# Kernel tuning notes

Measured on AMD Instinct MI355X. Metric: run time of the kernel, lower is better.

## Reference

```python
import jax, jax.numpy as jnp
import numpy as np

S, N, DIN, DH, C, K, E = 12, 50000, 64, 128, 2, 3, 600000
HID = (DH + C) // 2  # 65
LN_EPS = 1e-5


def setup_inputs() -> dict:
    key = jax.random.key(0)
    ks = jax.random.split(key, 16)
    sc = 0.05
    inp = {
        'H': jax.random.normal(ks[0], (S, N, DIN), dtype=jnp.float32),
        'edge_index': jax.random.randint(ks[1], (2, E), 0, N, dtype=jnp.int64),
        # stacked gate params, gate order: 0=i, 1=f, 2=c(cell), 3=o
        'Wx': jax.random.normal(ks[2], (4, K, DIN, DH), dtype=jnp.float32) * sc,
        'bx': jnp.zeros((4, DH), dtype=jnp.float32),
        'Wh': jax.random.normal(ks[3], (4, K, DH, DH), dtype=jnp.float32) * sc,
        'bh': jnp.zeros((4, DH), dtype=jnp.float32),
        'b_gate': jnp.zeros((4, DH), dtype=jnp.float32),
        'wc': jax.random.normal(ks[4], (3, DH), dtype=jnp.float32) * sc,  # peephole: i, f, o
        'ln_gamma': jnp.ones((DH,), dtype=jnp.float32),
        'ln_beta': jnp.zeros((DH,), dtype=jnp.float32),
        'W1': jax.random.normal(ks[5], (DH, HID), dtype=jnp.float32) * sc,
        'b1': jnp.zeros((HID,), dtype=jnp.float32),
        'W2': jax.random.normal(ks[6], (HID, C), dtype=jnp.float32) * sc,
        'b2': jnp.zeros((C,), dtype=jnp.float32),
    }
    return inp


def _cheb_norm(edge_index):
    # sym-normalized, lambda_max=2 => scaled Laplacian Lhat = -D^-1/2 A D^-1/2 (zero diagonal)
    src, dst = edge_index[0], edge_index[1]
    ones = jnp.ones((src.shape[0],), dtype=jnp.float32)
    deg = jax.ops.segment_sum(ones, src, num_segments=N)
    dinv = jnp.where(deg > 0, jax.lax.rsqrt(jnp.maximum(deg, 1.0)), 0.0)
    norm = -dinv[src] * dinv[dst]
    return src, dst, norm


def _cheb_conv(x, W, b, src, dst, norm):
    # x: [N, Din]; W: [K, Din, Dout]. T0=x, T1=Lhat x, Tk=2 Lhat T_{k-1} - T_{k-2}
    Tx0 = x
    out = Tx0 @ W[0]
    if K > 1:
        Tx1 = jax.ops.segment_sum(norm[:, None] * Tx0[src], dst, num_segments=N)
        out = out + Tx1 @ W[1]
        for k in range(2, K):
            Tx2 = 2.0 * jax.ops.segment_sum(norm[:, None] * Tx1[src], dst, num_segments=N) - Tx0
            out = out + Tx2 @ W[k]
            Tx0, Tx1 = Tx1, Tx2
    return out + b


def _decoder(H, edge_index, Wx, bx, Wh, bh, b_gate, wc, ln_gamma, ln_beta, W1, b1, W2, b2):
    src, dst, norm = _cheb_norm(edge_index)

    def step(carry, x_t):
        h, c = carry
        gx = lambda g: _cheb_conv(x_t, Wx[g], bx[g], src, dst, norm)
        gh = lambda g: _cheb_conv(h, Wh[g], bh[g], src, dst, norm)
        i = jax.nn.sigmoid(gx(0) + gh(0) + wc[0] * c + b_gate[0])
        f = jax.nn.sigmoid(gx(1) + gh(1) + wc[1] * c + b_gate[1])
        t = jnp.tanh(gx(2) + gh(2) + b_gate[2])
        c = f * c + i * t
        o = jax.nn.sigmoid(gx(3) + gh(3) + wc[2] * c + b_gate[3])
        h = o * jnp.tanh(c)
        return (h, c), h

    h0 = jnp.zeros((N, DH), dtype=H.dtype)
    (_, _), X = jax.lax.scan(step, (h0, h0), H)  # X: [S, N, DH]

    X = jnp.tanh(X)
    # LayerNorm over conv_dim (last axis here)
    mu = jnp.mean(X, axis=-1, keepdims=True)
    var = jnp.mean(jnp.square(X - mu), axis=-1, keepdims=True)
    X = (X - mu) * jax.lax.rsqrt(var + LN_EPS) * ln_gamma + ln_beta
    # dropout in eval mode: identity
    X = jax.nn.relu(X @ W1 + b1) @ W2 + b2  # [S, N, C]
    X = jax.nn.sigmoid(X)
    return jnp.transpose(X, (1, 2, 0))  # [N, C, S]


def reference(H, edge_index, Wx, bx, Wh, bh, b_gate, wc, ln_gamma, ln_beta, W1, b1, W2, b2):
    return _decoder(H, edge_index, Wx, bx, Wh, bh, b_gate, wc, ln_gamma, ln_beta, W1, b1, W2, b2)
```

## Files before the change

kernel.cpp:

```cpp
#include <hip/hip_runtime.h>
#include <cstdint>
#include <cstddef>

#define S_DIM 12
#define N_NODE 50000
#define N_PAD 50048
#define N_P2 50176
#define D_IN 64
#define D_H 128
#define N_E 600000
#define K_TOT 576
#define N_COL 512
#define HID_P 80
#define N_HID 65
#define AXC 192

#define NB_PREP 1152
#define NB_DEG 2344
#define NB_SPMM 12500
#define NB_LN 782

typedef short bf16x8 __attribute__((ext_vector_type(8)));
typedef float f32x4 __attribute__((ext_vector_type(4)));

__device__ __forceinline__ float bf2f(unsigned short u){
  union { unsigned int i; float f; } v; v.i = ((unsigned int)u) << 16; return v.f;
}
__device__ __forceinline__ unsigned short f2bf(float f){
  union { float f; unsigned int i; } v; v.f = f;
  unsigned int x = v.i;
  return (unsigned short)((x + 0x7fffu + ((x >> 16) & 1u)) >> 16);
}
__device__ __forceinline__ float sigf(float x){ return 1.f/(1.f + __expf(-x)); }
__device__ __forceinline__ float ftanh(float x){
  x = fminf(fmaxf(x, -12.f), 12.f);
  float e = __expf(2.f*x);
  return (e - 1.f)/(e + 1.f);
}
__device__ __forceinline__ void gload16(const void* g, void* lds){
  __builtin_amdgcn_global_load_lds((const __attribute__((address_space(1))) unsigned int*)g,
                                   (__attribute__((address_space(3))) unsigned int*)lds, 16, 0, 0);
}
__device__ __forceinline__ void acc6(float* a, unsigned int p0, unsigned int p1, unsigned int p2, float w){
  unsigned int u[3] = {p0, p1, p2};
#pragma unroll
  for (int i=0;i<3;++i){
    a[2*i]   += w * bf2f((unsigned short)(u[i] & 0xffffu));
    a[2*i+1] += w * bf2f((unsigned short)(u[i] >> 16));
  }
}
__device__ __forceinline__ void acc8(float* a, uint4 h, float w){
  unsigned int u[4] = {h.x, h.y, h.z, h.w};
#pragma unroll
  for (int i=0;i<4;++i){
    a[2*i]   += w * bf2f((unsigned short)(u[i] & 0xffffu));
    a[2*i+1] += w * bf2f((unsigned short)(u[i] >> 16));
  }
}

__global__ void k_setup(const int* __restrict__ ei,
                        const float* __restrict__ Wx, const float* __restrict__ Wh,
                        const float* __restrict__ bx, const float* __restrict__ bh,
                        const float* __restrict__ bg, const float* __restrict__ W1,
                        const float* __restrict__ b1, const float* __restrict__ W2,
                        unsigned short* __restrict__ Bct, float* __restrict__ btot,
                        unsigned short* __restrict__ W1t, float* __restrict__ b1p,
                        float* __restrict__ W2p,
                        int* __restrict__ dsrc, int* __restrict__ ddst)
{
  int bb = blockIdx.x, tid = threadIdx.x;
  if (bb < NB_PREP){
    int idx = bb*256 + tid;
    if (idx < N_COL*K_TOT){
      int cc = idx / K_TOT, k = idx - cc*K_TOT;
      int g = (cc>>4)&3, d = (cc&15) + ((cc>>6)<<4);
      float v;
      if (k < 384){
        int kt = k >> 7, j = k & 127;
        const float* Wg = Wh + (size_t)g*3*128*128;
        if (kt == 0)      v = Wg[(size_t)j*128 + d] - Wg[(size_t)(256+j)*128 + d];
        else if (kt == 1) v = Wg[(size_t)(128+j)*128 + d];
        else              v = 2.f*Wg[(size_t)(256+j)*128 + d];
      } else {
        int kk = k - 384; int kt = kk >> 6, j = kk & 63;
        const float* Wg = Wx + (size_t)g*3*64*128;
        if (kt == 0)      v = Wg[(size_t)j*128 + d] - Wg[(size_t)(128+j)*128 + d];
        else if (kt == 1) v = Wg[(size_t)(64+j)*128 + d];
        else              v = 2.f*Wg[(size_t)(128+j)*128 + d];
      }
      Bct[(size_t)cc*K_TOT + k] = f2bf(v);
    }
    if (idx < N_COL) btot[idx] = bx[idx] + bh[idx] + bg[idx];
    if (idx < HID_P*D_H){ int c = idx >> 7, k = idx & 127;
      W1t[idx] = (c < N_HID) ? f2bf(W1[k*N_HID + c]) : (unsigned short)0; }
    if (idx < HID_P) b1p[idx] = (idx < N_HID) ? b1[idx] : 0.f;
    if (idx < HID_P*2){ int c = idx >> 1, j = idx & 1; W2p[idx] = (c < N_HID) ? W2[c*2 + j] : 0.f; }
  } else {
    int e = (bb - NB_PREP)*256 + tid;
    if (e < N_E){
      atomicAdd(&dsrc[ei[e]], 1);
      atomicAdd(&ddst[ei[N_E + e]], 1);
    }
  }
}

__global__ void k_xprep(const float* __restrict__ H, unsigned short* __restrict__ Xtr,
                        unsigned short* __restrict__ Axt)
{
  int idx = blockIdx.x*256 + threadIdx.x;
  if (idx >= N_PAD*32) return;
  int n = idx >> 5, d0 = (idx & 31)*2;
  unsigned int pk[12];
  if (n < N_NODE){
    const float* hp = H + (size_t)n*64 + d0;
#pragma unroll
    for (int t=0;t<12;++t){
      float2 v = *(const float2*)(hp + (size_t)t*N_NODE*64);
      pk[t] = (unsigned int)f2bf(v.x) | ((unsigned int)f2bf(v.y) << 16);
    }
  } else {
#pragma unroll
    for (int t=0;t<12;++t) pk[t] = 0;
  }
#pragma unroll
  for (int t=0;t<12;++t)
    *(unsigned int*)(Axt + ((size_t)t*N_PAD + n)*AXC + d0) = pk[t];
  if (n >= N_NODE){
#pragma unroll
    for (int t=0;t<12;++t){
      *(unsigned int*)(Axt + ((size_t)t*N_PAD + n)*AXC + 64  + d0) = 0;
      *(unsigned int*)(Axt + ((size_t)t*N_PAD + n)*AXC + 128 + d0) = 0;
    }
  }
  unsigned int* c0  = (unsigned int*)(Xtr + ((size_t)n*64 + d0)*6);
  unsigned int* c1  = (unsigned int*)(Xtr + ((size_t)n*64 + d0 + 1)*6);
  unsigned int* c0b = (unsigned int*)(Xtr + (size_t)N_PAD*384 + ((size_t)n*64 + d0)*6);
  unsigned int* c1b = (unsigned int*)(Xtr + (size_t)N_PAD*384 + ((size_t)n*64 + d0 + 1)*6);
#pragma unroll
  for (int i=0;i<3;++i){
    c0[i]  = (pk[2*i]   & 0xffffu) | (pk[2*i+1]   << 16);
    c1[i]  = (pk[2*i]   >> 16)     | (pk[2*i+1]   & 0xffff0000u);
    c0b[i] = (pk[6+2*i] & 0xffffu) | (pk[6+2*i+1] << 16);
    c1b[i] = (pk[6+2*i] >> 16)     | (pk[6+2*i+1] & 0xffff0000u);
  }
}

__global__ void k_scan1d(const int* __restrict__ in, int* __restrict__ outp, int* __restrict__ part,
                         const int* __restrict__ dsrc, float* __restrict__ dinv){
  __shared__ int sm[256];
  int tid = threadIdx.x;
  int i = blockIdx.x*256 + tid;
  dinv[i] = (dsrc[i] > 0) ? rsqrtf((float)dsrc[i]) : 0.f;
  int v = in[i];
  int x = v;
  sm[tid] = x; __syncthreads();
  for (int off=1; off<256; off<<=1){
    int y = (tid >= off) ? sm[tid-off] : 0;
    __syncthreads();
    x += y; sm[tid] = x; __syncthreads();
  }
  outp[i] = x - v;
  if (tid == 255) part[blockIdx.x] = x;
}
__global__ void k_scan2(int* __restrict__ part, int nblk){
  __shared__ int sm[256];
  int tid = threadIdx.x;
  int v = (tid < nblk) ? part[tid] : 0;
  int x = v; sm[tid] = x; __syncthreads();
  for (int off=1; off<256; off<<=1){
    int y = (tid >= off) ? sm[tid-off] : 0;
    __syncthreads();
    x += y; sm[tid] = x; __syncthreads();
  }
  if (tid < nblk) part[tid] = x - v;
}
__global__ void k_scan3(const int* __restrict__ outp, const int* __restrict__ part, int* __restrict__ offs){
  int i = blockIdx.x*256 + threadIdx.x;
  offs[i] = outp[i] + part[blockIdx.x];
}
__global__ void k_csr(const int* __restrict__ ei, const float* __restrict__ dinv,
                      const int* __restrict__ offs, int* __restrict__ cursor,
                      int2* __restrict__ cedge){
  int e = blockIdx.x*256 + threadIdx.x;
  if (e < N_E){
    int s = ei[e], d = ei[N_E + e];
    int pos = atomicAdd(&cursor[d], 1);
    float w = -dinv[s]*dinv[d];
    cedge[offs[d] + pos] = make_int2(s, __float_as_int(w));
  }
}

__global__ void k_xspmm1(const unsigned short* __restrict__ Xh, unsigned short* __restrict__ AxtH,
                         unsigned short* __restrict__ Uh,
                         const int* __restrict__ offs, const int2* __restrict__ cedge){
  int n = blockIdx.x*4 + (threadIdx.x >> 6);
  int l = threadIdx.x & 63;
  if (n >= N_NODE) return;
  int beg = offs[n], end = offs[n+1];
  int ce = end - 1;
  float a[6];
#pragma unroll
  for (int t=0;t<6;++t) a[t] = 0.f;
  for (int q = beg; q < end; q += 6){
    int2 e0 = cedge[min(q,   ce)];
    int2 e1 = cedge[min(q+1, ce)];
    int2 e2 = cedge[min(q+2, ce)];
    int2 e3 = cedge[min(q+3, ce)];
    int2 e4 = cedge[min(q+4, ce)];
    int2 e5 = cedge[min(q+5, ce)];
    float w0 = __int_as_float(e0.y);
    float w1 = (q+1 < end) ? __int_as_float(e1.y) : 0.f;
    float w2 = (q+2 < end) ? __int_as_float(e2.y) : 0.f;
    float w3 = (q+3 < end) ? __int_as_float(e3.y) : 0.f;
    float w4 = (q+4 < end) ? __int_as_float(e4.y) : 0.f;
    float w5 = (q+5 < end) ? __int_as_float(e5.y) : 0.f;
    const unsigned int* r0 = (const unsigned int*)(Xh + ((size_t)e0.x*64 + l)*6);
    const unsigned int* r1 = (const unsigned int*)(Xh + ((size_t)e1.x*64 + l)*6);
    const unsigned int* r2 = (const unsigned int*)(Xh + ((size_t)e2.x*64 + l)*6);
    const unsigned int* r3 = (const unsigned int*)(Xh + ((size_t)e3.x*64 + l)*6);
    const unsigned int* r4 = (const unsigned int*)(Xh + ((size_t)e4.x*64 + l)*6);
    const unsigned int* r5 = (const unsigned int*)(Xh + ((size_t)e5.x*64 + l)*6);
    unsigned int p00=r0[0], p01=r0[1], p02=r0[2];
    unsigned int p10=r1[0], p11=r1[1], p12=r1[2];
    unsigned int p20=r2[0], p21=r2[1], p22=r2[2];
    unsigned int p30=r3[0], p31=r3[1], p32=r3[2];
    unsigned int p40=r4[0], p41=r4[1], p42=r4[2];
    unsigned int p50=r5[0], p51=r5[1], p52=r5[2];
    acc6(a, p00, p01, p02, w0);
    acc6(a, p10, p11, p12, w1);
    acc6(a, p20, p21, p22, w2);
    acc6(a, p30, p31, p32, w3);
    acc6(a, p40, p41, p42, w4);
    acc6(a, p50, p51, p52, w5);
  }
  unsigned short u[6];
#pragma unroll
  for (int t=0;t<6;++t){
    u[t] = f2bf(a[t]);
    AxtH[((size_t)t*N_PAD + n)*AXC + 64 + l] = u[t];
  }
  unsigned int* op = (unsigned int*)(Uh + ((size_t)n*64 + l)*6);
#pragma unroll
  for (int i=0;i<3;++i) op[i] = (unsigned int)u[2*i] | ((unsigned int)u[2*i+1] << 16);
}
__global__ void k_xspmm2(const unsigned short* __restrict__ Uh, unsigned short* __restrict__ AxtH,
                         const int* __restrict__ offs, const int2* __restrict__ cedge){
  int n = blockIdx.x*4 + (threadIdx.x >> 6);
  int l = threadIdx.x & 63;
  if (n >= N_NODE) return;
  int beg = offs[n], end = offs[n+1];
  int ce = end - 1;
  float a[6];
#pragma unroll
  for (int t=0;t<6;++t) a[t] = 0.f;
  for (int q = beg; q < end; q += 6){
    int2 e0 = cedge[min(q,   ce)];
    int2 e1 = cedge[min(q+1, ce)];
    int2 e2 = cedge[min(q+2, ce)];
    int2 e3 = cedge[min(q+3, ce)];
    int2 e4 = cedge[min(q+4, ce)];
    int2 e5 = cedge[min(q+5, ce)];
    float w0 = __int_as_float(e0.y);
    float w1 = (q+1 < end) ? __int_as_float(e1.y) : 0.f;
    float w2 = (q+2 < end) ? __int_as_float(e2.y) : 0.f;
    float w3 = (q+3 < end) ? __int_as_float(e3.y) : 0.f;
    float w4 = (q+4 < end) ? __int_as_float(e4.y) : 0.f;
    float w5 = (q+5 < end) ? __int_as_float(e5.y) : 0.f;
    const unsigned int* r0 = (const unsigned int*)(Uh + ((size_t)e0.x*64 + l)*6);
    const unsigned int* r1 = (const unsigned int*)(Uh + ((size_t)e1.x*64 + l)*6);
    const unsigned int* r2 = (const unsigned int*)(Uh + ((size_t)e2.x*64 + l)*6);
    const unsigned int* r3 = (const unsigned int*)(Uh + ((size_t)e3.x*64 + l)*6);
    const unsigned int* r4 = (const unsigned int*)(Uh + ((size_t)e4.x*64 + l)*6);
    const unsigned int* r5 = (const unsigned int*)(Uh + ((size_t)e5.x*64 + l)*6);
    unsigned int p00=r0[0], p01=r0[1], p02=r0[2];
    unsigned int p10=r1[0], p11=r1[1], p12=r1[2];
    unsigned int p20=r2[0], p21=r2[1], p22=r2[2];
    unsigned int p30=r3[0], p31=r3[1], p32=r3[2];
    unsigned int p40=r4[0], p41=r4[1], p42=r4[2];
    unsigned int p50=r5[0], p51=r5[1], p52=r5[2];
    acc6(a, p00, p01, p02, w0);
    acc6(a, p10, p11, p12, w1);
    acc6(a, p20, p21, p22, w2);
    acc6(a, p30, p31, p32, w3);
    acc6(a, p40, p41, p42, w4);
    acc6(a, p50, p51, p52, w5);
  }
#pragma unroll
  for (int t=0;t<6;++t)
    AxtH[((size_t)t*N_PAD + n)*AXC + 128 + l] = f2bf(a[t]);
}

__device__ __forceinline__ void spmm1_body(int n, int l,
    const unsigned short* __restrict__ Hc, unsigned short* __restrict__ U,
    const int* __restrict__ offs, const int2* __restrict__ cedge)
{
  if (n >= N_NODE) return;
  int sub = l >> 4, fl = l & 15;
  int beg = offs[n], end = offs[n+1];
  int ce = end - 1;
  float a[8];
#pragma unroll
  for (int j=0;j<8;++j) a[j] = 0.f;
  for (int q = beg; q < end; q += 16){
    int i0 = q + sub, i1 = q + 4 + sub, i2 = q + 8 + sub, i3 = q + 12 + sub;
    int2 e0 = cedge[min(i0, ce)];
    int2 e1 = cedge[min(i1, ce)];
    int2 e2 = cedge[min(i2, ce)];
    int2 e3 = cedge[min(i3, ce)];
    float w0 = (i0 < end) ? __int_as_float(e0.y) : 0.f;
    float w1 = (i1 < end) ? __int_as_float(e1.y) : 0.f;
    float w2 = (i2 < end) ? __int_as_float(e2.y) : 0.f;
    float w3 = (i3 < end) ? __int_as_float(e3.y) : 0.f;
    uint4 h0 = *(const uint4*)(Hc + (size_t)e0.x*128 + fl*8);
    uint4 h1 = *(const uint4*)(Hc + (size_t)e1.x*128 + fl*8);
    uint4 h2 = *(const uint4*)(Hc + (size_t)e2.x*128 + fl*8);
    uint4 h3 = *(const uint4*)(Hc + (size_t)e3.x*128 + fl*8);
    acc8(a, h0, w0);
    acc8(a, h1, w1);
    acc8(a, h2, w2);
    acc8(a, h3, w3);
  }
#pragma unroll
  for (int j=0;j<8;++j){
    a[j] += __shfl_xor(a[j], 16);
    a[j] += __shfl_xor(a[j], 32);
  }
  if (sub == 0){
    unsigned short o[8];
#pragma unroll
    for (int j=0;j<8;++j) o[j] = f2bf(a[j]);
    *(uint4*)(U + (size_t)n*256 + fl*8) = *(const uint4*)o;
  }
}

__global__ void k_spmm2(unsigned short* __restrict__ U,
                        const int* __restrict__ offs, const int2* __restrict__ cedge){
  int n = blockIdx.x*4 + (threadIdx.x >> 6);
  int l = threadIdx.x & 63;
  if (n >= N_NODE) return;
  int sub = l >> 4, fl = l & 15;
  int beg = offs[n], end = offs[n+1];
  int ce = end - 1;
  float a[8];
#pragma unroll
  for (int j=0;j<8;++j) a[j] = 0.f;
  for (int q = beg; q < end; q += 16){
    int i0 = q + sub, i1 = q + 4 + sub, i2 = q + 8 + sub, i3 = q + 12 + sub;
    int2 e0 = cedge[min(i0, ce)];
    int2 e1 = cedge[min(i1, ce)];
    int2 e2 = cedge[min(i2, ce)];
    int2 e3 = cedge[min(i3, ce)];
    float w0 = (i0 < end) ? __int_as_float(e0.y) : 0.f;
    float w1 = (i1 < end) ? __int_as_float(e1.y) : 0.f;
    float w2 = (i2 < end) ? __int_as_float(e2.y) : 0.f;
    float w3 = (i3 < end) ? __int_as_float(e3.y) : 0.f;
    uint4 h0 = *(const uint4*)(U + (size_t)e0.x*256 + fl*8);
    uint4 h1 = *(const uint4*)(U + (size_t)e1.x*256 + fl*8);
    uint4 h2 = *(const uint4*)(U + (size_t)e2.x*256 + fl*8);
    uint4 h3 = *(const uint4*)(U + (size_t)e3.x*256 + fl*8);
    acc8(a, h0, w0);
    acc8(a, h1, w1);
    acc8(a, h2, w2);
    acc8(a, h3, w3);
  }
#pragma unroll
  for (int j=0;j<8;++j){
    a[j] += __shfl_xor(a[j], 16);
    a[j] += __shfl_xor(a[j], 32);
  }
  if (sub == 0){
    unsigned short o[8];
#pragma unroll
    for (int j=0;j<8;++j) o[j] = f2bf(a[j]);
    *(uint4*)(U + (size_t)n*256 + 128 + fl*8) = *(const uint4*)o;
  }
}

__device__ __forceinline__ void lnmlp_body(int n0,
    const unsigned short* __restrict__ Hn,
    const unsigned short* __restrict__ W1t, const float* __restrict__ b1p,
    const float* __restrict__ W2p, const float* __restrict__ b2,
    const float* __restrict__ gam, const float* __restrict__ bet,
    float* __restrict__ out, int t)
{
  __shared__ __align__(16) unsigned short xn[64*128];
  __shared__ __align__(16) unsigned short w1s[HID_P*128];
  __shared__ float w2s[HID_P*2];
  __shared__ float b1s[HID_P];
  __shared__ float b2s[2];
  int tid = threadIdx.x;
  for (int i = tid; i < HID_P*128/8; i += 256) ((int4*)w1s)[i] = ((const int4*)W1t)[i];
  if (tid < HID_P*2) w2s[tid] = W2p[tid];
  if (tid < HID_P)   b1s[tid] = b1p[tid];
  if (tid < 2)       b2s[tid] = b2[tid];
  int row = tid >> 2, part = tid & 3;
  int n = n0 + row;
  float vals[32];
  float s = 0.f, ss = 0.f;
  if (n < N_NODE){
    const unsigned short* hp = Hn + (size_t)n*128 + part*32;
#pragma unroll
    for (int k=0;k<32;++k){
      float x = ftanh(bf2f(hp[k]));
      vals[k] = x; s += x; ss += x*x;
    }
  } else {
#pragma unroll
    for (int k=0;k<32;++k) vals[k] = 0.f;
  }
  s  += __shfl_xor(s,1);  s  += __shfl_xor(s,2);
  ss += __shfl_xor(ss,1); ss += __shfl_xor(ss,2);
  float mu = s * (1.f/128.f);
  float var = ss * (1.f/128.f) - mu*mu;
  float inv = rsqrtf(fmaxf(var, 0.f) + 1e-5f);
#pragma unroll
  for (int k=0;k<32;++k){
    int d = part*32 + k;
    xn[row*128 + d] = f2bf((vals[k]-mu)*inv*gam[d] + bet[d]);
  }
  __syncthreads();
  int w = tid >> 6, l = tid & 63;
  const f32x4 vzero = {0.f,0.f,0.f,0.f};
  f32x4 acc[5];
#pragma unroll
  for (int tj=0;tj<5;++tj) acc[tj] = vzero;
#pragma unroll
  for (int kk=0;kk<4;++kk){
    bf16x8 a = *(const bf16x8*)(xn + (w*16 + (l&15))*128 + kk*32 + (l>>4)*8);
#pragma unroll
    for (int tj=0;tj<5;++tj){
      bf16x8 b = *(const bf16x8*)(w1s + (tj*16 + (l&15))*128 + kk*32 + (l>>4)*8);
      acc[tj] = __builtin_amdgcn_mfma_f32_16x16x32_bf16(a, b, acc[tj], 0,0,0);
    }
  }
#pragma unroll
  for (int r=0;r<4;++r){
    int rn = n0 + w*16 + (l>>4)*4 + r;
    float p0 = 0.f, p1 = 0.f;
#pragma unroll
    for (int tj=0;tj<5;++tj){
      int col = tj*16 + (l&15);
      float hv = fmaxf(acc[tj][r] + b1s[col], 0.f);
      p0 += hv * w2s[col*2];
      p1 += hv * w2s[col*2+1];
    }
    p0 += __shfl_xor(p0,1); p0 += __shfl_xor(p0,2); p0 += __shfl_xor(p0,4); p0 += __shfl_xor(p0,8);
    p1 += __shfl_xor(p1,1); p1 += __shfl_xor(p1,2); p1 += __shfl_xor(p1,4); p1 += __shfl_xor(p1,8);
    if ((l & 15) == 0 && rn < N_NODE){
      float* op = out + (size_t)rn*24 + t;
      op[0]  = sigf(p0 + b2s[0]);
      op[12] = sigf(p1 + b2s[1]);
    }
  }
}

__global__ void k_sp1ln(const unsigned short* __restrict__ Hc, unsigned short* __restrict__ U,
                        const int* __restrict__ offs, const int2* __restrict__ cedge,
                        const unsigned short* __restrict__ W1t, const float* __restrict__ b1p,
                        const float* __restrict__ W2p, const float* __restrict__ b2,
                        const float* __restrict__ gam, const float* __restrict__ bet,
                        float* __restrict__ out, int tprev)
{
  int bb = blockIdx.x;
  if (bb < NB_SPMM){
    spmm1_body(bb*4 + (threadIdx.x >> 6), threadIdx.x & 63, Hc, U, offs, cedge);
  } else {
    lnmlp_body((bb - NB_SPMM)*64, Hc, W1t, b1p, W2p, b2, gam, bet, out, tprev);
  }
}

__global__ __launch_bounds__(256,2) void k_lnmlp(const unsigned short* __restrict__ Hn,
                        const unsigned short* __restrict__ W1t, const float* __restrict__ b1p,
                        const float* __restrict__ W2p, const float* __restrict__ b2,
                        const float* __restrict__ gam, const float* __restrict__ bet,
                        float* __restrict__ out, int t)
{
  lnmlp_body(blockIdx.x*64, Hn, W1t, b1p, W2p, b2, gam, bet, out, t);
}

__global__ __launch_bounds__(256,3) void k_gemm(
    const unsigned short* __restrict__ Hc, const unsigned short* __restrict__ U,
    const unsigned short* __restrict__ Axt,
    const unsigned short* __restrict__ Bct, const float* __restrict__ btot,
    const float* __restrict__ wc, float* __restrict__ c, unsigned short* __restrict__ Hn,
    int it0)
{
  int L = blockIdx.y*4 + blockIdx.x;
  int xcd = L & 7, li = L >> 3;
  int by = xcd + ((li >> 2) << 3);
  int bx = li & 3;
  if (by >= N_PAD/128) return;
  __shared__ __align__(16) unsigned short As[128*64];
  __shared__ __align__(16) unsigned short Bs[128*64];
  int tid = threadIdx.x;
  int w = tid >> 6, l = tid & 63;
  int n0 = bx * 128;
  int m0 = by * 128;
  const f32x4 vzero = {0.f,0.f,0.f,0.f};
  f32x4 acc[4][4];
#pragma unroll
  for (int i=0;i<4;++i)
#pragma unroll
    for (int j=0;j<4;++j) acc[i][j] = vzero;
  int wr = w >> 1, wn = w & 1;
  for (int it=it0; it<9; ++it){
    const unsigned short* Ab; int astr, acol;
    if (it < 2)      { Ab = Hc;  astr = 128; acol = it*64; }
    else if (it < 6) { Ab = U;   astr = 256; acol = (it-2)*64; }
    else             { Ab = Axt; astr = AXC; acol = (it-6)*64; }
    if (it != it0) __syncthreads();
#pragma unroll
    for (int i=0;i<4;++i){
      int rr = w*32 + i*8;
      int row = rr + (l>>3);
      gload16(Ab  + (size_t)(m0+row)*astr + acol + (l&7)*8, (void*)(As + rr*64));
      gload16(Bct + (size_t)(n0+row)*K_TOT + it*64 + (l&7)*8, (void*)(Bs + rr*64));
    }
    __syncthreads();
#pragma unroll
    for (int kk=0; kk<2; ++kk){
      bf16x8 af[4], bfv[4];
#pragma unroll
      for (int i=0;i<4;++i) af[i]  = *(const bf16x8*)(As + (wr*64 + i*16 + (l&15))*64 + kk*32 + (l>>4)*8);
#pragma unroll
      for (int j=0;j<4;++j) bfv[j] = *(const bf16x8*)(Bs + (wn*64 + j*16 + (l&15))*64 + kk*32 + (l>>4)*8);
#pragma unroll
      for (int i=0;i<4;++i)
#pragma unroll
        for (int j=0;j<4;++j)
          acc[i][j] = __builtin_amdgcn_mfma_f32_16x16x32_bf16(af[i], bfv[j], acc[i][j], 0,0,0);
    }
  }
  int dd = (((bx<<1) + wn) << 4) | (l & 15);
  float b_i = btot[dd], b_f = btot[128+dd], b_t = btot[256+dd], b_o = btot[384+dd];
  float wci = wc[dd], wcf = wc[128+dd], wco = wc[256+dd];
#pragma unroll
  for (int i=0;i<4;++i){
    int row0 = m0 + wr*64 + i*16 + (l>>4)*4;
#pragma unroll
    for (int r=0;r<4;++r){
      int row = row0 + r;
      float co = c[(size_t)row*128 + dd];
      float gi = sigf(acc[i][0][r] + b_i + wci*co);
      float gf = sigf(acc[i][1][r] + b_f + wcf*co);
      float tt = ftanh(acc[i][2][r] + b_t);
      float cn = gf*co + gi*tt;
      float go = sigf(acc[i][3][r] + b_o + wco*cn);
      float h = go * ftanh(cn);
      c[(size_t)row*128 + dd] = cn;
      Hn[(size_t)row*128 + dd] = f2bf(h);
    }
  }
}

extern "C" void kernel_launch(void* const* d_in, const int* in_sizes, int n_in,
                              void* d_out, int out_size, void* d_ws, size_t ws_size,
                              hipStream_t stream)
{
  const float* H   = (const float*)d_in[0];
  const int*   ei  = (const int*)d_in[1];
  const float* Wx  = (const float*)d_in[2];
  const float* bx  = (const float*)d_in[3];
  const float* Wh  = (const float*)d_in[4];
  const float* bh  = (const float*)d_in[5];
  const float* bg  = (const float*)d_in[6];
  const float* wc  = (const float*)d_in[7];
  const float* gam = (const float*)d_in[8];
  const float* bet = (const float*)d_in[9];
  const float* W1  = (const float*)d_in[10];
  const float* b1  = (const float*)d_in[11];
  const float* W2  = (const float*)d_in[12];
  const float* b2  = (const float*)d_in[13];
  float* out = (float*)d_out;
  (void)in_sizes; (void)n_in; (void)out_size; (void)ws_size;

  char* p = (char*)d_ws;
  auto alloc = [&](size_t bytes)->char*{ char* r = p; p += (bytes + 255) & ~(size_t)255; return r; };
  char* zbase = p;
  float* c_st  = (float*)alloc((size_t)N_PAD*128*4);
  int* dsrc   = (int*)alloc((size_t)N_P2*4);
  int* ddst   = (int*)alloc((size_t)N_P2*4);
  int* cursor = (int*)alloc((size_t)N_P2*4);
  size_t zbytes = (size_t)(p - zbase);
  unsigned short* Hbuf0 = (unsigned short*)alloc((size_t)N_PAD*128*2);
  unsigned short* Hbuf1 = (unsigned short*)alloc((size_t)N_PAD*128*2);
  unsigned short* Ubuf  = (unsigned short*)alloc((size_t)N_PAD*256*2);
  unsigned short* Xtr   = (unsigned short*)alloc((size_t)N_PAD*768*2);
  unsigned short* U1tr  = (unsigned short*)alloc((size_t)N_PAD*768*2);
  unsigned short* Axt   = (unsigned short*)alloc((size_t)S_DIM*N_PAD*AXC*2);
  unsigned short* Bct   = (unsigned short*)alloc((size_t)N_COL*K_TOT*2);
  float*          btot  = (float*)alloc(N_COL*4);
  unsigned short* W1t   = (unsigned short*)alloc(HID_P*128*2);
  float*          b1p   = (float*)alloc(HID_P*4);
  float*          W2p   = (float*)alloc(HID_P*2*4);
  float*          dinv  = (float*)alloc((size_t)N_P2*4);
  int*            offs  = (int*)alloc((size_t)(N_P2+256)*4);
  int*            outp  = (int*)alloc((size_t)N_P2*4);
  int*            partb = (int*)alloc(256*4);
  int2*           cedge = (int2*)alloc((size_t)N_E*8);

  hipMemsetAsync(zbase, 0, zbytes, stream);
  k_setup<<<NB_PREP + NB_DEG, 256, 0, stream>>>(ei, Wx, Wh, bx, bh, bg,
      W1, b1, W2, Bct, btot, W1t, b1p, W2p, dsrc, ddst);
  k_xprep<<<(N_PAD*32 + 255)/256, 256, 0, stream>>>(H, Xtr, Axt);
  k_scan1d<<<N_P2/256, 256, 0, stream>>>(ddst, outp, partb, dsrc, dinv);
  k_scan2<<<1, 256, 0, stream>>>(partb, N_P2/256);
  k_scan3<<<N_P2/256, 256, 0, stream>>>(outp, partb, offs);
  k_csr<<<NB_DEG, 256, 0, stream>>>(ei, dinv, offs, cursor, cedge);
  for (int h = 0; h < 2; ++h){
    k_xspmm1<<<NB_SPMM, 256, 0, stream>>>(Xtr + (size_t)h*N_PAD*384,
        Axt + (size_t)h*6*N_PAD*AXC, U1tr + (size_t)h*N_PAD*384, offs, cedge);
  }
  for (int h = 0; h < 2; ++h){
    k_xspmm2<<<NB_SPMM, 256, 0, stream>>>(U1tr + (size_t)h*N_PAD*384,
        Axt + (size_t)h*6*N_PAD*AXC, offs, cedge);
  }

  k_gemm<<<dim3(4, 392), 256, 0, stream>>>(Hbuf0, Ubuf, Axt,
      Bct, btot, wc, c_st, Hbuf1, 6);
  for (int t = 1; t < S_DIM; ++t){
    unsigned short* Hc = (t & 1) ? Hbuf1 : Hbuf0;
    unsigned short* Hn = (t & 1) ? Hbuf0 : Hbuf1;
    k_sp1ln<<<NB_SPMM + NB_LN, 256, 0, stream>>>(Hc, Ubuf, offs, cedge,
        W1t, b1p, W2p, b2, gam, bet, out, t-1);
    k_spmm2<<<NB_SPMM, 256, 0, stream>>>(Ubuf, offs, cedge);
    k_gemm<<<dim3(4, 392), 256, 0, stream>>>(Hc, Ubuf,
        Axt + (size_t)t*N_PAD*AXC, Bct, btot, wc, c_st, Hn, 0);
  }
  k_lnmlp<<<NB_LN, 256, 0, stream>>>(Hbuf0, W1t, b1p, W2p, b2, gam, bet, out, 11);
}
```

Measured before the change: 1.864 ms.

## Stage xprep through LDS, fuse scan kernels, merge half launches, store cell state bf16

k_xprep now loads H with float4 reads, stages the bf16 values in shared memory and writes the interleaved Xtr layout from there, replacing strided scattered stores. The two small scan kernels are merged into one, and the per-half xspmm launches become single launches with twice the blocks. The LSTM cell state is stored as bf16 instead of fp32 and prefetched before the GEMM main loop, which halves its memory traffic at the cost of precision. Block order in the spmm/LN fused kernel is also swapped so the LN blocks are dispatched first.

After: 1.905 ms. 1.02x slower.

```diff
diff --git a/kernel.cpp b/kernel.cpp
--- a/kernel.cpp
+++ b/kernel.cpp
@@ -104,44 +104,56 @@
   }
 }
 
-__global__ void k_xprep(const float* __restrict__ H, unsigned short* __restrict__ Xtr,
-                        unsigned short* __restrict__ Axt)
-{
-  int idx = blockIdx.x*256 + threadIdx.x;
-  if (idx >= N_PAD*32) return;
-  int n = idx >> 5, d0 = (idx & 31)*2;
-  unsigned int pk[12];
-  if (n < N_NODE){
-    const float* hp = H + (size_t)n*64 + d0;
-#pragma unroll
-    for (int t=0;t<12;++t){
-      float2 v = *(const float2*)(hp + (size_t)t*N_NODE*64);
-      pk[t] = (unsigned int)f2bf(v.x) | ((unsigned int)f2bf(v.y) << 16);
-    }
-  } else {
-#pragma unroll
-    for (int t=0;t<12;++t) pk[t] = 0;
-  }
-#pragma unroll
-  for (int t=0;t<12;++t)
-    *(unsigned int*)(Axt + ((size_t)t*N_PAD + n)*AXC + d0) = pk[t];
-  if (n >= N_NODE){
-#pragma unroll
-    for (int t=0;t<12;++t){
-      *(unsigned int*)(Axt + ((size_t)t*N_PAD + n)*AXC + 64  + d0) = 0;
-      *(unsigned int*)(Axt + ((size_t)t*N_PAD + n)*AXC + 128 + d0) = 0;
-    }
-  }
-  unsigned int* c0  = (unsigned int*)(Xtr + ((size_t)n*64 + d0)*6);
-  unsigned int* c1  = (unsigned int*)(Xtr + ((size_t)n*64 + d0 + 1)*6);
-  unsigned int* c0b = (unsigned int*)(Xtr + (size_t)N_PAD*384 + ((size_t)n*64 + d0)*6);
-  unsigned int* c1b = (unsigned int*)(Xtr + (size_t)N_PAD*384 + ((size_t)n*64 + d0 + 1)*6);
-#pragma unroll
-  for (int i=0;i<3;++i){
-    c0[i]  = (pk[2*i]   & 0xffffu) | (pk[2*i+1]   << 16);
-    c1[i]  = (pk[2*i]   >> 16)     | (pk[2*i+1]   & 0xffff0000u);
-    c0b[i] = (pk[6+2*i] & 0xffffu) | (pk[6+2*i+1] << 16);
-    c1b[i] = (pk[6+2*i] >> 16)     | (pk[6+2*i+1] & 0xffff0000u);
+#define XP_STR 2056
+__global__ __launch_bounds__(256,3) void k_xprep(const float* __restrict__ H,
+                        unsigned short* __restrict__ Xtr, unsigned short* __restrict__ Axt)
+{
+  __shared__ unsigned short xls[12*XP_STR];
+  int bb = blockIdx.x, tid = threadIdx.x;
+  int n0 = bb*32;
+  int nn = tid >> 3;
+  int d  = (tid & 7)*8;
+  int gn = n0 + nn;
+#pragma unroll
+  for (int t=0;t<12;++t){
+    unsigned short u[8];
+    if (gn < N_NODE){
+      const float* hp = H + ((size_t)t*N_NODE + gn)*64 + d;
+      float4 a = *(const float4*)hp;
+      float4 b = *(const float4*)(hp+4);
+      u[0]=f2bf(a.x); u[1]=f2bf(a.y); u[2]=f2bf(a.z); u[3]=f2bf(a.w);
+      u[4]=f2bf(b.x); u[5]=f2bf(b.y); u[6]=f2bf(b.z); u[7]=f2bf(b.w);
+    } else {
+#pragma unroll
+      for (int i=0;i<8;++i) u[i]=0;
+    }
+    *(int4*)(xls + t*XP_STR + nn*64 + d) = *(const int4*)u;
+    *(int4*)(Axt + ((size_t)t*N_PAD + gn)*AXC + d) = *(const int4*)u;
+    if (gn >= N_NODE){
+      *(int4*)(Axt + ((size_t)t*N_PAD + gn)*AXC + 64 + d)  = *(const int4*)u;
+      *(int4*)(Axt + ((size_t)t*N_PAD + gn)*AXC + 128 + d) = *(const int4*)u;
+    }
+  }
+  __syncthreads();
+#pragma unroll
+  for (int rep=0; rep<8; ++rep){
+    int cIdx = rep*256 + tid;
+    int n = cIdx >> 6, dd = cIdx & 63;
+    unsigned int w0[3], w1[3];
+#pragma unroll
+    for (int i=0;i<3;++i){
+      unsigned short a0 = xls[(2*i  )*XP_STR + n*64 + dd];
+      unsigned short a1 = xls[(2*i+1)*XP_STR + n*64 + dd];
+      unsigned short b0 = xls[(6+2*i)*XP_STR + n*64 + dd];
+      unsigned short b1 = xls[(7+2*i)*XP_STR + n*64 + dd];
+      w0[i] = (unsigned int)a0 | ((unsigned int)a1<<16);
+      w1[i] = (unsigned int)b0 | ((unsigned int)b1<<16);
+    }
+    size_t cell = ((size_t)(n0+n)*64 + dd)*6;
+    unsigned int* p0 = (unsigned int*)(Xtr + cell);
+    unsigned int* p1 = (unsigned int*)(Xtr + (size_t)N_PAD*384 + cell);
+    p0[0]=w0[0]; p0[1]=w0[1]; p0[2]=w0[2];
+    p1[0]=w1[0]; p1[1]=w1[1]; p1[2]=w1[2];
   }
 }
 
@@ -162,21 +174,20 @@
   outp[i] = x - v;
   if (tid == 255) part[blockIdx.x] = x;
 }
-__global__ void k_scan2(int* __restrict__ part, int nblk){
+__global__ void k_scan3f(const int* __restrict__ outp, const int* __restrict__ part,
+                         int* __restrict__ offs){
   __shared__ int sm[256];
   int tid = threadIdx.x;
-  int v = (tid < nblk) ? part[tid] : 0;
+  int v = (tid < N_P2/256) ? part[tid] : 0;
   int x = v; sm[tid] = x; __syncthreads();
   for (int off=1; off<256; off<<=1){
     int y = (tid >= off) ? sm[tid-off] : 0;
     __syncthreads();
     x += y; sm[tid] = x; __syncthreads();
   }
-  if (tid < nblk) part[tid] = x - v;
-}
-__global__ void k_scan3(const int* __restrict__ outp, const int* __restrict__ part, int* __restrict__ offs){
-  int i = blockIdx.x*256 + threadIdx.x;
-  offs[i] = outp[i] + part[blockIdx.x];
+  int pref = (blockIdx.x > 0) ? sm[blockIdx.x - 1] : 0;
+  int i = blockIdx.x*256 + tid;
+  offs[i] = outp[i] + pref;
 }
 __global__ void k_csr(const int* __restrict__ ei, const float* __restrict__ dinv,
                       const int* __restrict__ offs, int* __restrict__ cursor,
@@ -190,10 +201,15 @@
   }
 }
 
-__global__ void k_xspmm1(const unsigned short* __restrict__ Xh, unsigned short* __restrict__ AxtH,
-                         unsigned short* __restrict__ Uh,
+__global__ void k_xspmm1(const unsigned short* __restrict__ Xtr, unsigned short* __restrict__ Axt,
+                         unsigned short* __restrict__ U1tr,
                          const int* __restrict__ offs, const int2* __restrict__ cedge){
-  int n = blockIdx.x*4 + (threadIdx.x >> 6);
+  int bb = blockIdx.x;
+  int h = (bb >= NB_SPMM) ? 1 : 0;
+  const unsigned short* Xh = Xtr + (size_t)h*N_PAD*384;
+  unsigned short* AxtH = Axt + (size_t)h*6*N_PAD*AXC;
+  unsigned short* Uh = U1tr + (size_t)h*N_PAD*384;
+  int n = (bb - h*NB_SPMM)*4 + (threadIdx.x >> 6);
   int l = threadIdx.x & 63;
   if (n >= N_NODE) return;
   int beg = offs[n], end = offs[n+1];
@@ -243,9 +259,13 @@
 #pragma unroll
   for (int i=0;i<3;++i) op[i] = (unsigned int)u[2*i] | ((unsigned int)u[2*i+1] << 16);
 }
-__global__ void k_xspmm2(const unsigned short* __restrict__ Uh, unsigned short* __restrict__ AxtH,
+__global__ void k_xspmm2(const unsigned short* __restrict__ U1tr, unsigned short* __restrict__ Axt,
                          const int* __restrict__ offs, const int2* __restrict__ cedge){
-  int n = blockIdx.x*4 + (threadIdx.x >> 6);
+  int bb = blockIdx.x;
+  int h = (bb >= NB_SPMM) ? 1 : 0;
+  const unsigned short* Uh = U1tr + (size_t)h*N_PAD*384;
+  unsigned short* AxtH = Axt + (size_t)h*6*N_PAD*AXC;
+  int n = (bb - h*NB_SPMM)*4 + (threadIdx.x >> 6);
   int l = threadIdx.x & 63;
   if (n >= N_NODE) return;
   int beg = offs[n], end = offs[n+1];
@@ -462,10 +482,10 @@
                         float* __restrict__ out, int tprev)
 {
   int bb = blockIdx.x;
-  if (bb < NB_SPMM){
-    spmm1_body(bb*4 + (threadIdx.x >> 6), threadIdx.x & 63, Hc, U, offs, cedge);
+  if (bb < NB_LN){
+    lnmlp_body(bb*64, Hc, W1t, b1p, W2p, b2, gam, bet, out, tprev);
   } else {
-    lnmlp_body((bb - NB_SPMM)*64, Hc, W1t, b1p, W2p, b2, gam, bet, out, tprev);
+    spmm1_body((bb - NB_LN)*4 + (threadIdx.x >> 6), threadIdx.x & 63, Hc, U, offs, cedge);
   }
 }
 
@@ -482,8 +502,8 @@
     const unsigned short* __restrict__ Hc, const unsigned short* __restrict__ U,
     const unsigned short* __restrict__ Axt,
     const unsigned short* __restrict__ Bct, const float* __restrict__ btot,
-    const float* __restrict__ wc, float* __restrict__ c, unsigned short* __restrict__ Hn,
-    int it0)
+    const float* __restrict__ wc, unsigned short* __restrict__ cst,
+    unsigned short* __restrict__ Hn, int it0)
 {
   int L = blockIdx.y*4 + blockIdx.x;
   int xcd = L & 7, li = L >> 3;
@@ -496,13 +516,24 @@
   int w = tid >> 6, l = tid & 63;
   int n0 = bx * 128;
   int m0 = by * 128;
+  int wr = w >> 1, wn = w & 1;
+  int dd = (((bx<<1) + wn) << 4) | (l & 15);
+  float cof[4][4];
+#pragma unroll
+  for (int i=0;i<4;++i)
+#pragma unroll
+    for (int r=0;r<4;++r){
+      int row = m0 + wr*64 + i*16 + (l>>4)*4 + r;
+      cof[i][r] = bf2f(cst[(size_t)row*128 + dd]);
+    }
+  float b_i = btot[dd], b_f = btot[128+dd], b_t = btot[256+dd], b_o = btot[384+dd];
+  float wci = wc[dd], wcf = wc[128+dd], wco = wc[256+dd];
   const f32x4 vzero = {0.f,0.f,0.f,0.f};
   f32x4 acc[4][4];
 #pragma unroll
   for (int i=0;i<4;++i)
 #pragma unroll
     for (int j=0;j<4;++j) acc[i][j] = vzero;
-  int wr = w >> 1, wn = w & 1;
   for (int it=it0; it<9; ++it){
     const unsigned short* Ab; int astr, acol;
     if (it < 2)      { Ab = Hc;  astr = 128; acol = it*64; }
@@ -531,23 +562,20 @@
           acc[i][j] = __builtin_amdgcn_mfma_f32_16x16x32_bf16(af[i], bfv[j], acc[i][j], 0,0,0);
     }
   }
-  int dd = (((bx<<1) + wn) << 4) | (l & 15);
-  float b_i = btot[dd], b_f = btot[128+dd], b_t = btot[256+dd], b_o = btot[384+dd];
-  float wci = wc[dd], wcf = wc[128+dd], wco = wc[256+dd];
 #pragma unroll
   for (int i=0;i<4;++i){
     int row0 = m0 + wr*64 + i*16 + (l>>4)*4;
 #pragma unroll
     for (int r=0;r<4;++r){
       int row = row0 + r;
-      float co = c[(size_t)row*128 + dd];
+      float co = cof[i][r];
       float gi = sigf(acc[i][0][r] + b_i + wci*co);
       float gf = sigf(acc[i][1][r] + b_f + wcf*co);
       float tt = ftanh(acc[i][2][r] + b_t);
       float cn = gf*co + gi*tt;
       float go = sigf(acc[i][3][r] + b_o + wco*cn);
       float h = go * ftanh(cn);
-      c[(size_t)row*128 + dd] = cn;
+      cst[(size_t)row*128 + dd] = f2bf(cn);
       Hn[(size_t)row*128 + dd] = f2bf(h);
     }
   }
@@ -577,7 +605,7 @@
   char* p = (char*)d_ws;
   auto alloc = [&](size_t bytes)->char*{ char* r = p; p += (bytes + 255) & ~(size_t)255; return r; };
   char* zbase = p;
-  float* c_st  = (float*)alloc((size_t)N_PAD*128*4);
+  unsigned short* c_st = (unsigned short*)alloc((size_t)N_PAD*128*2);
   int* dsrc   = (int*)alloc((size_t)N_P2*4);
   int* ddst   = (int*)alloc((size_t)N_P2*4);
   int* cursor = (int*)alloc((size_t)N_P2*4);
@@ -602,19 +630,12 @@
   hipMemsetAsync(zbase, 0, zbytes, stream);
   k_setup<<<NB_PREP + NB_DEG, 256, 0, stream>>>(ei, Wx, Wh, bx, bh, bg,
       W1, b1, W2, Bct, btot, W1t, b1p, W2p, dsrc, ddst);
-  k_xprep<<<(N_PAD*32 + 255)/256, 256, 0, stream>>>(H, Xtr, Axt);
+  k_xprep<<<N_PAD/32, 256, 0, stream>>>(H, Xtr, Axt);
   k_scan1d<<<N_P2/256, 256, 0, stream>>>(ddst, outp, partb, dsrc, dinv);
-  k_scan2<<<1, 256, 0, stream>>>(partb, N_P2/256);
-  k_scan3<<<N_P2/256, 256, 0, stream>>>(outp, partb, offs);
+  k_scan3f<<<N_P2/256, 256, 0, stream>>>(outp, partb, offs);
   k_csr<<<NB_DEG, 256, 0, stream>>>(ei, dinv, offs, cursor, cedge);
-  for (int h = 0; h < 2; ++h){
-    k_xspmm1<<<NB_SPMM, 256, 0, stream>>>(Xtr + (size_t)h*N_PAD*384,
-        Axt + (size_t)h*6*N_PAD*AXC, U1tr + (size_t)h*N_PAD*384, offs, cedge);
-  }
-  for (int h = 0; h < 2; ++h){
-    k_xspmm2<<<NB_SPMM, 256, 0, stream>>>(U1tr + (size_t)h*N_PAD*384,
-        Axt + (size_t)h*6*N_PAD*AXC, offs, cedge);
-  }
+  k_xspmm1<<<2*NB_SPMM, 256, 0, stream>>>(Xtr, Axt, U1tr, offs, cedge);
+  k_xspmm2<<<2*NB_SPMM, 256, 0, stream>>>(U1tr, Axt, offs, cedge);
 
   k_gemm<<<dim3(4, 392), 256, 0, stream>>>(Hbuf0, Ubuf, Axt,
       Bct, btot, wc, c_st, Hbuf1, 6);
```
